# Optimization experiments

Measured on AMD Instinct MI355X. Metric: run time of the kernel, lower is better.

The kernel has to match this reference:

```python
import jax, jax.numpy as jnp
import numpy as np


def _normalize_xyz_with_pc(pc, xyz):
    # Center by point-cloud centroid, scale by max radius of centered cloud.
    center = pc.mean(axis=1, keepdims=True)                      # [B,1,3]
    pc_c = pc - center
    scale = jnp.sqrt((pc_c ** 2).sum(-1)).max(axis=1)            # [B]
    scale = jnp.maximum(scale, 1e-6)[:, None, None]              # [B,1,1]
    return (xyz - center) / scale


def _nn_gather(seed_n, pts_n, feat):
    # seed_n [B,M,3], pts_n [B,K,3], feat [B,C,K] -> [B,C,M]
    d2 = ((seed_n ** 2).sum(-1)[:, :, None]
          + (pts_n ** 2).sum(-1)[:, None, :]
          - 2.0 * jnp.einsum('bmd,bkd->bmk', seed_n, pts_n))     # [B,M,K]
    idx = jnp.argmin(d2, axis=-1)                                # [B,M]
    return jnp.take_along_axis(feat, idx[:, None, :], axis=2)    # [B,C,M]


def _conv1x1(w, b, x):
    # w [O,C], b [O], x [B,C,M] -> [B,O,M]
    return jnp.einsum('oc,bcm->bom', w, x) + b[None, :, None]


def setup_inputs() -> dict:
    key = jax.random.key(0)
    ks = jax.random.split(key, 10)
    B, N, M, K, D = 4, 20000, 1024, 16384, 768
    return {
        'point_cloud': jax.random.normal(ks[0], (B, N, 3), jnp.float32),
        'seed_xyz': jax.random.normal(ks[1], (B, M, 3), jnp.float32),
        'seed_features': jax.random.normal(ks[2], (B, 256, M), jnp.float32),
        'pts': jax.random.normal(ks[3], (B, K, 3), jnp.float32),
        'feat': jax.random.normal(ks[4], (B, D, K), jnp.float32),
        'ln_gamma': jnp.ones((D,), jnp.float32),
        'ln_beta': jnp.zeros((D,), jnp.float32),
        'pw1': jax.random.normal(ks[5], (256, D), jnp.float32) * 0.02,
        'pb1': jnp.zeros((256,), jnp.float32),
        'pw2': jax.random.normal(ks[6], (256, 256), jnp.float32) * 0.02,
        'pb2': jnp.zeros((256,), jnp.float32),
        'fw1': jax.random.normal(ks[7], (256, 512), jnp.float32) * 0.02,
        'fb1': jnp.zeros((256,), jnp.float32),
        'fw2': jax.random.normal(ks[8], (256, 256), jnp.float32) * 0.02,
        'fb2': jnp.zeros((256,), jnp.float32),
    }


def reference(point_cloud, seed_xyz, seed_features, pts, feat,
              ln_gamma, ln_beta, pw1, pb1, pw2, pb2, fw1, fb1, fw2, fb2):
    seed_n = _normalize_xyz_with_pc(point_cloud, seed_xyz)       # [B,M,3]
    pts_n = _normalize_xyz_with_pc(point_cloud, pts)             # [B,K,3]
    vggt_raw = _nn_gather(seed_n, pts_n, feat)                   # [B,768,M]

    # LayerNorm over channel dim (applied on [B,M,768] in the original)
    x = vggt_raw.transpose(0, 2, 1)                              # [B,M,768]
    mu = x.mean(-1, keepdims=True)
    var = x.var(-1, keepdims=True)
    x_ln = ((x - mu) * jax.lax.rsqrt(var + 1e-5) * ln_gamma + ln_beta)
    x_ln = x_ln.transpose(0, 2, 1)                               # [B,768,M]

    vggt_proj = _conv1x1(pw2, pb2, jax.nn.relu(_conv1x1(pw1, pb1, x_ln)))
    fused = jnp.concatenate([seed_features, vggt_proj], axis=1)  # [B,512,M]
    mixed = _conv1x1(fw2, fb2, jax.nn.relu(_conv1x1(fw1, fb1, fused)))
    return mixed                                                 # [B,256,M]
```

## Files before the change

### kernel.cpp

```cpp
#include <hip/hip_runtime.h>
#include <math.h>

#define B_ 4
#define N_ 20000
#define M_ 1024
#define K_ 16384
#define D_ 768

typedef __attribute__((ext_vector_type(8))) short bf16x8;
typedef __attribute__((ext_vector_type(4))) float f32x4;

#define OFF_PART   0ul
#define OFF_RAD    1024ul
#define OFF_IDX    4096ul
#define OFF_P4     32768ul
#define OFF_G      2097152ul
#define OFF_XLN    16777216ul
#define OFF_FUSED  25165824ul
#define OFF_H2     29360128ul
#define OFF_WB1    33554432ul
#define OFF_WCAT   34603008ul
#define OFF_WB4    35651584ul
#define OFF_BC     36700160ul

__device__ inline unsigned short f2bf(float x) {
    union { float f; unsigned int u; } v; v.f = x;
    unsigned int r = v.u + 0x7fffu + ((v.u >> 16) & 1u);
    return (unsigned short)(r >> 16);
}

__device__ inline void gload_lds16(const void* g, void* lds) {
    __builtin_amdgcn_global_load_lds(
        (const __attribute__((address_space(1))) unsigned int*)g,
        (__attribute__((address_space(3))) unsigned int*)lds, 16, 0, 0);
}

__global__ __launch_bounds__(256) void k_cs_sum(const float* __restrict__ pc,
                                                float* __restrict__ part)
{
    int blk = blockIdx.x, b = blk >> 4, pi = blk & 15;
    const float* p = pc + (size_t)b * N_ * 3;
    int tid = threadIdx.x;
    int i0 = pi * 1250;
    float sx = 0.f, sy = 0.f, sz = 0.f;
    for (int i = i0 + tid; i < i0 + 1250; i += 256) {
        sx += p[i*3+0]; sy += p[i*3+1]; sz += p[i*3+2];
    }
    for (int off = 32; off; off >>= 1) {
        sx += __shfl_down(sx, off, 64);
        sy += __shfl_down(sy, off, 64);
        sz += __shfl_down(sz, off, 64);
    }
    __shared__ float red[3][4];
    int w = tid >> 6, l = tid & 63;
    if (!l) { red[0][w] = sx; red[1][w] = sy; red[2][w] = sz; }
    __syncthreads();
    if (!tid) {
        part[(b*16+pi)*3+0] = red[0][0]+red[0][1]+red[0][2]+red[0][3];
        part[(b*16+pi)*3+1] = red[1][0]+red[1][1]+red[1][2]+red[1][3];
        part[(b*16+pi)*3+2] = red[2][0]+red[2][1]+red[2][2]+red[2][3];
    }
}

__device__ inline void reduce_center(const float* part, int b,
                                     float& cx, float& cy, float& cz)
{
    cx = 0.f; cy = 0.f; cz = 0.f;
    #pragma unroll
    for (int r = 0; r < 16; ++r) {
        cx += part[(b*16+r)*3+0];
        cy += part[(b*16+r)*3+1];
        cz += part[(b*16+r)*3+2];
    }
    cx *= (1.f/N_); cy *= (1.f/N_); cz *= (1.f/N_);
}

__global__ __launch_bounds__(256) void k_cs_rad(const float* __restrict__ pc,
                                                const float* __restrict__ part,
                                                float* __restrict__ rad)
{
    int blk = blockIdx.x, b = blk >> 4, pi = blk & 15;
    float cx, cy, cz;
    reduce_center(part, b, cx, cy, cz);
    const float* p = pc + (size_t)b * N_ * 3;
    int tid = threadIdx.x;
    int i0 = pi * 1250;
    float mx = 0.f;
    for (int i = i0 + tid; i < i0 + 1250; i += 256) {
        float dx = p[i*3+0]-cx, dy = p[i*3+1]-cy, dz = p[i*3+2]-cz;
        mx = fmaxf(mx, dx*dx + dy*dy + dz*dz);
    }
    for (int off = 32; off; off >>= 1) mx = fmaxf(mx, __shfl_down(mx, off, 64));
    __shared__ float red[4];
    int w = tid >> 6, l = tid & 63;
    if (!l) red[w] = mx;
    __syncthreads();
    if (!tid) rad[b*16+pi] = fmaxf(fmaxf(red[0], red[1]), fmaxf(red[2], red[3]));
}

__device__ inline float reduce_scale(const float* rad, int b)
{
    float m = 0.f;
    #pragma unroll
    for (int r = 0; r < 16; ++r) m = fmaxf(m, rad[b*16+r]);
    return fmaxf(sqrtf(m), 1e-6f);
}

__global__ __launch_bounds__(256) void k_prep_pts(const float* __restrict__ pts,
                                                  const float* __restrict__ part,
                                                  const float* __restrict__ rad,
                                                  float4* __restrict__ P4)
{
    int blk = blockIdx.x, b = blk >> 6;
    float cx, cy, cz;
    reduce_center(part, b, cx, cy, cz);
    float sc = 1.f / reduce_scale(rad, b);
    int k = (blk & 63)*256 + threadIdx.x;
    const float* pp = pts + ((size_t)b*K_ + k)*3;
    float px = (pp[0]-cx)*sc, py = (pp[1]-cy)*sc, pz = (pp[2]-cz)*sc;
    P4[(size_t)b*K_ + k] = make_float4(px, py, pz, px*px + py*py + pz*pz);
}

__global__ __launch_bounds__(256) void k_nn(const float* __restrict__ seed_xyz,
                                            const float4* __restrict__ P4,
                                            const float* __restrict__ part,
                                            const float* __restrict__ rad,
                                            int* __restrict__ idx)
{
    int blk = blockIdx.x, b = blk >> 7, g = blk & 127;
    float cx, cy, cz;
    reduce_center(part, b, cx, cy, cz);
    float sc = 1.f / reduce_scale(rad, b);
    int t = threadIdx.x;
    int j = t & 31, s = t >> 5;
    int m = g*8 + s;
    const float* sp = seed_xyz + ((size_t)b*M_ + m)*3;
    float sx = (sp[0]-cx)*sc, sy = (sp[1]-cy)*sc, sz = (sp[2]-cz)*sc;
    float ssq = sx*sx + sy*sy + sz*sz;
    const float4* Pb = P4 + (size_t)b*K_;

    float best[4] = {3.4e38f, 3.4e38f, 3.4e38f, 3.4e38f};
    int   bk[4]   = {0, 0, 0, 0};
    for (int i = 0; i < 512; i += 4) {
        #pragma unroll
        for (int r = 0; r < 4; ++r) {
            int k = (i + r)*32 + j;
            float4 q = Pb[k];
            float d2 = ssq + q.w - 2.f*(sx*q.x + sy*q.y + sz*q.z);
            if (d2 < best[r]) { best[r] = d2; bk[r] = k; }
        }
    }
    float bm = best[0]; int bmk = bk[0];
    #pragma unroll
    for (int r = 1; r < 4; ++r) {
        if (best[r] < bm || (best[r] == bm && bk[r] < bmk)) { bm = best[r]; bmk = bk[r]; }
    }
    #pragma unroll
    for (int mask = 16; mask; mask >>= 1) {
        float ob = __shfl_xor(bm, mask, 64);
        int   ok = __shfl_xor(bmk, mask, 64);
        if (ob < bm || (ob == bm && ok < bmk)) { bm = ob; bmk = ok; }
    }
    if (j == 0) idx[b*M_ + m] = bmk;
}

__global__ __launch_bounds__(256) void k_gather(const float* __restrict__ feat,
                                                const int* __restrict__ idx,
                                                float* __restrict__ G)
{
    int c = blockIdx.x, b = blockIdx.y;
    int t = threadIdx.x;
    const float* frow = feat + ((size_t)b*D_ + c) * K_;
    const int* ib = idx + b*M_;
    float* grow = G + ((size_t)b*D_ + c) * M_;
    #pragma unroll
    for (int r = 0; r < 4; ++r) {
        int m = r*256 + t;
        grow[m] = frow[ib[m]];
    }
}

__global__ __launch_bounds__(256) void k_ln_fused(const float* __restrict__ G,
                                                  const float* __restrict__ gamma,
                                                  const float* __restrict__ beta,
                                                  unsigned short* __restrict__ xln)
{
    int b = blockIdx.y, m0 = blockIdx.x * 32;
    int t = threadIdx.x;
    int ml = t & 31, cp = t >> 5;
    const float* Gb = G + (size_t)b * D_ * M_;
    float s = 0.f, q = 0.f;
    for (int c = cp; c < D_; c += 8) {
        float v = Gb[(size_t)c*M_ + m0 + ml];
        s += v; q += v*v;
    }
    __shared__ float sred[8][32], qred[8][32];
    __shared__ float mu[32], iv[32];
    sred[cp][ml] = s; qred[cp][ml] = q;
    __syncthreads();
    if (t < 32) {
        float S = 0.f, Q = 0.f;
        #pragma unroll
        for (int r = 0; r < 8; ++r) { S += sred[r][t]; Q += qred[r][t]; }
        float m_ = S * (1.f/768.f);
        mu[t] = m_;
        iv[t] = rsqrtf(Q * (1.f/768.f) - m_*m_ + 1e-5f);
    }
    __syncthreads();

    __shared__ float tile[64][33];
    int ty = t >> 5;
    int cx2 = t & 31;
    for (int c0 = 0; c0 < D_; c0 += 64) {
        __syncthreads();
        #pragma unroll
        for (int ri = 0; ri < 8; ++ri) {
            int cl = ty*8 + ri;
            tile[cl][ml] = Gb[(size_t)(c0+cl)*M_ + m0 + ml];
        }
        __syncthreads();
        float2 ga = *(const float2*)&gamma[c0 + 2*cx2];
        float2 be = *(const float2*)&beta[c0 + 2*cx2];
        #pragma unroll
        for (int ri = 0; ri < 4; ++ri) {
            int m_l = ty*4 + ri;
            float v0 = (tile[2*cx2+0][m_l] - mu[m_l]) * iv[m_l] * ga.x + be.x;
            float v1 = (tile[2*cx2+1][m_l] - mu[m_l]) * iv[m_l] * ga.y + be.y;
            ushort2 pk = make_ushort2(f2bf(v0), f2bf(v1));
            *(ushort2*)&xln[((size_t)((b<<10) + m0 + m_l))*D_ + c0 + 2*cx2] = pk;
        }
    }
}

__global__ void k_transpose_sf(const float* __restrict__ sf,
                               unsigned short* __restrict__ fused)
{
    __shared__ float tile[32][33];
    int m0 = blockIdx.x*32, c0 = blockIdx.y*32, b = blockIdx.z;
    int tx = threadIdx.x, ty = threadIdx.y;
    #pragma unroll
    for (int r = 0; r < 32; r += 8)
        tile[ty+r][tx] = sf[((size_t)b*256 + c0+ty+r)*M_ + m0 + tx];
    __syncthreads();
    #pragma unroll
    for (int r = 0; r < 32; r += 8)
        fused[((size_t)(b*M_ + m0+ty+r))*512 + c0 + tx] = f2bf(tile[tx][ty+r]);
}

__global__ __launch_bounds__(256) void k_cvt(const float* __restrict__ pw1,
                                             const float* __restrict__ fw1,
                                             const float* __restrict__ fw2,
                                             unsigned short* __restrict__ Wb1,
                                             unsigned short* __restrict__ Wcat,
                                             unsigned short* __restrict__ Wb4)
{
    int i = blockIdx.x*256 + threadIdx.x;
    Wb1[i] = f2bf(pw1[i]);
    if (i < 65536) {
        int o = i >> 8, c = i & 255;
        Wcat[(size_t)o*512 + c] = f2bf(fw1[(size_t)o*512 + c]);
        Wb4[i] = f2bf(fw2[i]);
    }
}

__global__ __launch_bounds__(256) void k_wc(const float* __restrict__ fw1,
                                            const float* __restrict__ pw2,
                                            const float* __restrict__ pb2,
                                            const float* __restrict__ fb1,
                                            unsigned short* __restrict__ Wcat,
                                            float* __restrict__ bc)
{
    int o = blockIdx.x, t = threadIdx.x;
    const float* fb = fw1 + (size_t)o*512 + 256;
    float acc = 0.f;
    for (int j = 0; j < 256; ++j)
        acc = fmaf(fb[j], pw2[(size_t)j*256 + t], acc);
    Wcat[(size_t)o*512 + 256 + t] = f2bf(acc);
    float v = fb[t] * pb2[t];
    for (int off = 32; off; off >>= 1) v += __shfl_down(v, off, 64);
    __shared__ float red[4];
    if (!(t & 63)) red[t >> 6] = v;
    __syncthreads();
    if (!t) bc[o] = red[0]+red[1]+red[2]+red[3] + fb1[o];
}

__global__ __launch_bounds__(256) void k_gemm_mfma(
    const unsigned short* __restrict__ X, const unsigned short* __restrict__ W,
    const float* __restrict__ bias, int Kdim, int relu, int mode,
    unsigned short* __restrict__ Ybf, int rowStride, int colOff,
    float* __restrict__ Yf)
{
    __shared__ unsigned short Al[64*64];
    __shared__ unsigned short Wl[64*64];
    int t = threadIdx.x, l = t & 63, w = t >> 6;
    int m0 = blockIdx.x * 64, o0 = blockIdx.y * 64;
    f32x4 acc[4];
    #pragma unroll
    for (int j = 0; j < 4; ++j) acc[j] = (f32x4){0.f, 0.f, 0.f, 0.f};

    for (int kc = 0; kc < Kdim; kc += 64) {
        #pragma unroll
        for (int i = 0; i < 2; ++i) {
            int lin = i*4096 + w*1024;
            int lb  = lin + l*16;
            int row = lb >> 7;
            int k16 = (lb >> 4) & 7;
            int ks  = k16 ^ (row & 7);
            gload_lds16(X + (size_t)(m0+row)*Kdim + kc + ks*8, (char*)Al + lin);
            gload_lds16(W + (size_t)(o0+row)*Kdim + kc + ks*8, (char*)Wl + lin);
        }
        __syncthreads();
        #pragma unroll
        for (int kk = 0; kk < 2; ++kk) {
            int arow = w*16 + (l & 15);
            int h = l >> 4;
            bf16x8 a = *(const bf16x8*)&Al[arow*64 + (((kk<<2)|h) ^ (arow & 7))*8];
            #pragma unroll
            for (int j = 0; j < 4; ++j) {
                int orow = j*16 + (l & 15);
                bf16x8 bfr = *(const bf16x8*)&Wl[orow*64 + (((kk<<2)|h) ^ (orow & 7))*8];
                acc[j] = __builtin_amdgcn_mfma_f32_16x16x32_bf16(a, bfr, acc[j], 0, 0, 0);
            }
        }
        __syncthreads();
    }

    int mbase = m0 + w*16 + (l >> 4)*4;
    if (mode == 0) {
        #pragma unroll
        for (int j = 0; j < 4; ++j) {
            int o = o0 + j*16 + (l & 15);
            float bi = bias[o];
            #pragma unroll
            for (int r = 0; r < 4; ++r) {
                float v = acc[j][r] + bi;
                if (relu) v = fmaxf(v, 0.f);
                Ybf[(size_t)(mbase + r)*rowStride + colOff + o] = f2bf(v);
            }
        }
    } else {
        int b = mbase >> 10, ml = mbase & 1023;
        #pragma unroll
        for (int j = 0; j < 4; ++j) {
            int o = o0 + j*16 + (l & 15);
            float bi = bias[o];
            float4 sv = make_float4(acc[j][0]+bi, acc[j][1]+bi, acc[j][2]+bi, acc[j][3]+bi);
            *(float4*)&Yf[((size_t)(b*256 + o))*1024 + ml] = sv;
        }
    }
}

extern "C" void kernel_launch(void* const* d_in, const int* in_sizes, int n_in,
                              void* d_out, int out_size, void* d_ws, size_t ws_size,
                              hipStream_t stream)
{
    (void)in_sizes; (void)n_in; (void)out_size; (void)ws_size;
    const float* pc        = (const float*)d_in[0];
    const float* seed_xyz  = (const float*)d_in[1];
    const float* seed_feat = (const float*)d_in[2];
    const float* pts       = (const float*)d_in[3];
    const float* feat      = (const float*)d_in[4];
    const float* ln_g      = (const float*)d_in[5];
    const float* ln_b      = (const float*)d_in[6];
    const float* pw1       = (const float*)d_in[7];
    const float* pb1       = (const float*)d_in[8];
    const float* pw2       = (const float*)d_in[9];
    const float* pb2       = (const float*)d_in[10];
    const float* fw1       = (const float*)d_in[11];
    const float* fb1       = (const float*)d_in[12];
    const float* fw2       = (const float*)d_in[13];
    const float* fb2       = (const float*)d_in[14];
    float* out = (float*)d_out;

    char* ws = (char*)d_ws;
    float*          part  = (float*)(ws + OFF_PART);
    float*          rad   = (float*)(ws + OFF_RAD);
    int*            idx   = (int*)(ws + OFF_IDX);
    float4*         P4    = (float4*)(ws + OFF_P4);
    float*          G     = (float*)(ws + OFF_G);
    unsigned short* xln   = (unsigned short*)(ws + OFF_XLN);
    unsigned short* fused = (unsigned short*)(ws + OFF_FUSED);
    unsigned short* h2    = (unsigned short*)(ws + OFF_H2);
    unsigned short* Wb1   = (unsigned short*)(ws + OFF_WB1);
    unsigned short* Wcat  = (unsigned short*)(ws + OFF_WCAT);
    unsigned short* Wb4   = (unsigned short*)(ws + OFF_WB4);
    float*          bc    = (float*)(ws + OFF_BC);

    k_cvt<<<768, 256, 0, stream>>>(pw1, fw1, fw2, Wb1, Wcat, Wb4);
    k_wc<<<256, 256, 0, stream>>>(fw1, pw2, pb2, fb1, Wcat, bc);
    k_cs_sum<<<64, 256, 0, stream>>>(pc, part);
    k_cs_rad<<<64, 256, 0, stream>>>(pc, part, rad);
    k_prep_pts<<<256, 256, 0, stream>>>(pts, part, rad, P4);
    k_nn<<<512, 256, 0, stream>>>(seed_xyz, P4, part, rad, idx);
    k_gather<<<dim3(D_, B_), 256, 0, stream>>>(feat, idx, G);
    k_ln_fused<<<dim3(M_/32, B_), 256, 0, stream>>>(G, ln_g, ln_b, xln);
    k_gemm_mfma<<<dim3(64, 4), 256, 0, stream>>>(xln, Wb1, pb1, 768, 1, 0, fused, 512, 256, nullptr);
    k_transpose_sf<<<dim3(M_/32, 256/32, B_), dim3(32, 8), 0, stream>>>(seed_feat, fused);
    k_gemm_mfma<<<dim3(64, 4), 256, 0, stream>>>(fused, Wcat, bc, 512, 1, 0, h2, 256, 0, nullptr);
    k_gemm_mfma<<<dim3(64, 4), 256, 0, stream>>>(h2, Wb4, fb2, 256, 0, 1, nullptr, 0, 0, out);
}
```

Measured before the change: 164.7 us.

## Merge all stages into one cooperative persistent kernel with grid syncs

Result: slower. 345.2 us (+109.6%).

```diff
diff --git a/kernel.cpp b/kernel.cpp
--- a/kernel.cpp
+++ b/kernel.cpp
@@ -1,5 +1,8 @@
 #include <hip/hip_runtime.h>
+#include <hip/hip_cooperative_groups.h>
 #include <math.h>
+
+namespace cg = cooperative_groups;
 
 #define B_ 4
 #define N_ 20000
@@ -13,7 +16,6 @@
 #define OFF_PART   0ul
 #define OFF_RAD    1024ul
 #define OFF_IDX    4096ul
-#define OFF_P4     32768ul
 #define OFF_G      2097152ul
 #define OFF_XLN    16777216ul
 #define OFF_FUSED  25165824ul
@@ -35,32 +37,13 @@
         (__attribute__((address_space(3))) unsigned int*)lds, 16, 0, 0);
 }
 
-__global__ __launch_bounds__(256) void k_cs_sum(const float* __restrict__ pc,
-                                                float* __restrict__ part)
-{
-    int blk = blockIdx.x, b = blk >> 4, pi = blk & 15;
-    const float* p = pc + (size_t)b * N_ * 3;
-    int tid = threadIdx.x;
-    int i0 = pi * 1250;
-    float sx = 0.f, sy = 0.f, sz = 0.f;
-    for (int i = i0 + tid; i < i0 + 1250; i += 256) {
-        sx += p[i*3+0]; sy += p[i*3+1]; sz += p[i*3+2];
-    }
-    for (int off = 32; off; off >>= 1) {
-        sx += __shfl_down(sx, off, 64);
-        sy += __shfl_down(sy, off, 64);
-        sz += __shfl_down(sz, off, 64);
-    }
-    __shared__ float red[3][4];
-    int w = tid >> 6, l = tid & 63;
-    if (!l) { red[0][w] = sx; red[1][w] = sy; red[2][w] = sz; }
-    __syncthreads();
-    if (!tid) {
-        part[(b*16+pi)*3+0] = red[0][0]+red[0][1]+red[0][2]+red[0][3];
-        part[(b*16+pi)*3+1] = red[1][0]+red[1][1]+red[1][2]+red[1][3];
-        part[(b*16+pi)*3+2] = red[2][0]+red[2][1]+red[2][2]+red[2][3];
-    }
-}
+struct MegaArgs {
+    const float *pc, *seed_xyz, *sf, *pts, *feat, *ln_g, *ln_b;
+    const float *pw1, *pb1, *pw2, *pb2, *fw1, *fb1, *fw2, *fb2;
+    float *part; float *rad; int *idx; float *G;
+    unsigned short *xln, *fused, *h2, *Wb1, *Wcat, *Wb4;
+    float *bc; float *out;
+};
 
 __device__ inline void reduce_center(const float* part, int b,
                                      float& cx, float& cy, float& cz)
@@ -75,29 +58,6 @@
     cx *= (1.f/N_); cy *= (1.f/N_); cz *= (1.f/N_);
 }
 
-__global__ __launch_bounds__(256) void k_cs_rad(const float* __restrict__ pc,
-                                                const float* __restrict__ part,
-                                                float* __restrict__ rad)
-{
-    int blk = blockIdx.x, b = blk >> 4, pi = blk & 15;
-    float cx, cy, cz;
-    reduce_center(part, b, cx, cy, cz);
-    const float* p = pc + (size_t)b * N_ * 3;
-    int tid = threadIdx.x;
-    int i0 = pi * 1250;
-    float mx = 0.f;
-    for (int i = i0 + tid; i < i0 + 1250; i += 256) {
-        float dx = p[i*3+0]-cx, dy = p[i*3+1]-cy, dz = p[i*3+2]-cz;
-        mx = fmaxf(mx, dx*dx + dy*dy + dz*dz);
-    }
-    for (int off = 32; off; off >>= 1) mx = fmaxf(mx, __shfl_down(mx, off, 64));
-    __shared__ float red[4];
-    int w = tid >> 6, l = tid & 63;
-    if (!l) red[w] = mx;
-    __syncthreads();
-    if (!tid) rad[b*16+pi] = fmaxf(fmaxf(red[0], red[1]), fmaxf(red[2], red[3]));
-}
-
 __device__ inline float reduce_scale(const float* rad, int b)
 {
     float m = 0.f;
@@ -106,194 +66,15 @@
     return fmaxf(sqrtf(m), 1e-6f);
 }
 
-__global__ __launch_bounds__(256) void k_prep_pts(const float* __restrict__ pts,
-                                                  const float* __restrict__ part,
-                                                  const float* __restrict__ rad,
-                                                  float4* __restrict__ P4)
-{
-    int blk = blockIdx.x, b = blk >> 6;
-    float cx, cy, cz;
-    reduce_center(part, b, cx, cy, cz);
-    float sc = 1.f / reduce_scale(rad, b);
-    int k = (blk & 63)*256 + threadIdx.x;
-    const float* pp = pts + ((size_t)b*K_ + k)*3;
-    float px = (pp[0]-cx)*sc, py = (pp[1]-cy)*sc, pz = (pp[2]-cz)*sc;
-    P4[(size_t)b*K_ + k] = make_float4(px, py, pz, px*px + py*py + pz*pz);
-}
-
-__global__ __launch_bounds__(256) void k_nn(const float* __restrict__ seed_xyz,
-                                            const float4* __restrict__ P4,
-                                            const float* __restrict__ part,
-                                            const float* __restrict__ rad,
-                                            int* __restrict__ idx)
-{
-    int blk = blockIdx.x, b = blk >> 7, g = blk & 127;
-    float cx, cy, cz;
-    reduce_center(part, b, cx, cy, cz);
-    float sc = 1.f / reduce_scale(rad, b);
-    int t = threadIdx.x;
-    int j = t & 31, s = t >> 5;
-    int m = g*8 + s;
-    const float* sp = seed_xyz + ((size_t)b*M_ + m)*3;
-    float sx = (sp[0]-cx)*sc, sy = (sp[1]-cy)*sc, sz = (sp[2]-cz)*sc;
-    float ssq = sx*sx + sy*sy + sz*sz;
-    const float4* Pb = P4 + (size_t)b*K_;
-
-    float best[4] = {3.4e38f, 3.4e38f, 3.4e38f, 3.4e38f};
-    int   bk[4]   = {0, 0, 0, 0};
-    for (int i = 0; i < 512; i += 4) {
-        #pragma unroll
-        for (int r = 0; r < 4; ++r) {
-            int k = (i + r)*32 + j;
-            float4 q = Pb[k];
-            float d2 = ssq + q.w - 2.f*(sx*q.x + sy*q.y + sz*q.z);
-            if (d2 < best[r]) { best[r] = d2; bk[r] = k; }
-        }
-    }
-    float bm = best[0]; int bmk = bk[0];
-    #pragma unroll
-    for (int r = 1; r < 4; ++r) {
-        if (best[r] < bm || (best[r] == bm && bk[r] < bmk)) { bm = best[r]; bmk = bk[r]; }
-    }
-    #pragma unroll
-    for (int mask = 16; mask; mask >>= 1) {
-        float ob = __shfl_xor(bm, mask, 64);
-        int   ok = __shfl_xor(bmk, mask, 64);
-        if (ob < bm || (ob == bm && ok < bmk)) { bm = ob; bmk = ok; }
-    }
-    if (j == 0) idx[b*M_ + m] = bmk;
-}
-
-__global__ __launch_bounds__(256) void k_gather(const float* __restrict__ feat,
-                                                const int* __restrict__ idx,
-                                                float* __restrict__ G)
-{
-    int c = blockIdx.x, b = blockIdx.y;
-    int t = threadIdx.x;
-    const float* frow = feat + ((size_t)b*D_ + c) * K_;
-    const int* ib = idx + b*M_;
-    float* grow = G + ((size_t)b*D_ + c) * M_;
-    #pragma unroll
-    for (int r = 0; r < 4; ++r) {
-        int m = r*256 + t;
-        grow[m] = frow[ib[m]];
-    }
-}
-
-__global__ __launch_bounds__(256) void k_ln_fused(const float* __restrict__ G,
-                                                  const float* __restrict__ gamma,
-                                                  const float* __restrict__ beta,
-                                                  unsigned short* __restrict__ xln)
-{
-    int b = blockIdx.y, m0 = blockIdx.x * 32;
-    int t = threadIdx.x;
-    int ml = t & 31, cp = t >> 5;
-    const float* Gb = G + (size_t)b * D_ * M_;
-    float s = 0.f, q = 0.f;
-    for (int c = cp; c < D_; c += 8) {
-        float v = Gb[(size_t)c*M_ + m0 + ml];
-        s += v; q += v*v;
-    }
-    __shared__ float sred[8][32], qred[8][32];
-    __shared__ float mu[32], iv[32];
-    sred[cp][ml] = s; qred[cp][ml] = q;
-    __syncthreads();
-    if (t < 32) {
-        float S = 0.f, Q = 0.f;
-        #pragma unroll
-        for (int r = 0; r < 8; ++r) { S += sred[r][t]; Q += qred[r][t]; }
-        float m_ = S * (1.f/768.f);
-        mu[t] = m_;
-        iv[t] = rsqrtf(Q * (1.f/768.f) - m_*m_ + 1e-5f);
-    }
-    __syncthreads();
-
-    __shared__ float tile[64][33];
-    int ty = t >> 5;
-    int cx2 = t & 31;
-    for (int c0 = 0; c0 < D_; c0 += 64) {
-        __syncthreads();
-        #pragma unroll
-        for (int ri = 0; ri < 8; ++ri) {
-            int cl = ty*8 + ri;
-            tile[cl][ml] = Gb[(size_t)(c0+cl)*M_ + m0 + ml];
-        }
-        __syncthreads();
-        float2 ga = *(const float2*)&gamma[c0 + 2*cx2];
-        float2 be = *(const float2*)&beta[c0 + 2*cx2];
-        #pragma unroll
-        for (int ri = 0; ri < 4; ++ri) {
-            int m_l = ty*4 + ri;
-            float v0 = (tile[2*cx2+0][m_l] - mu[m_l]) * iv[m_l] * ga.x + be.x;
-            float v1 = (tile[2*cx2+1][m_l] - mu[m_l]) * iv[m_l] * ga.y + be.y;
-            ushort2 pk = make_ushort2(f2bf(v0), f2bf(v1));
-            *(ushort2*)&xln[((size_t)((b<<10) + m0 + m_l))*D_ + c0 + 2*cx2] = pk;
-        }
-    }
-}
-
-__global__ void k_transpose_sf(const float* __restrict__ sf,
-                               unsigned short* __restrict__ fused)
-{
-    __shared__ float tile[32][33];
-    int m0 = blockIdx.x*32, c0 = blockIdx.y*32, b = blockIdx.z;
-    int tx = threadIdx.x, ty = threadIdx.y;
-    #pragma unroll
-    for (int r = 0; r < 32; r += 8)
-        tile[ty+r][tx] = sf[((size_t)b*256 + c0+ty+r)*M_ + m0 + tx];
-    __syncthreads();
-    #pragma unroll
-    for (int r = 0; r < 32; r += 8)
-        fused[((size_t)(b*M_ + m0+ty+r))*512 + c0 + tx] = f2bf(tile[tx][ty+r]);
-}
-
-__global__ __launch_bounds__(256) void k_cvt(const float* __restrict__ pw1,
-                                             const float* __restrict__ fw1,
-                                             const float* __restrict__ fw2,
-                                             unsigned short* __restrict__ Wb1,
-                                             unsigned short* __restrict__ Wcat,
-                                             unsigned short* __restrict__ Wb4)
-{
-    int i = blockIdx.x*256 + threadIdx.x;
-    Wb1[i] = f2bf(pw1[i]);
-    if (i < 65536) {
-        int o = i >> 8, c = i & 255;
-        Wcat[(size_t)o*512 + c] = f2bf(fw1[(size_t)o*512 + c]);
-        Wb4[i] = f2bf(fw2[i]);
-    }
-}
-
-__global__ __launch_bounds__(256) void k_wc(const float* __restrict__ fw1,
-                                            const float* __restrict__ pw2,
-                                            const float* __restrict__ pb2,
-                                            const float* __restrict__ fb1,
-                                            unsigned short* __restrict__ Wcat,
-                                            float* __restrict__ bc)
-{
-    int o = blockIdx.x, t = threadIdx.x;
-    const float* fb = fw1 + (size_t)o*512 + 256;
-    float acc = 0.f;
-    for (int j = 0; j < 256; ++j)
-        acc = fmaf(fb[j], pw2[(size_t)j*256 + t], acc);
-    Wcat[(size_t)o*512 + 256 + t] = f2bf(acc);
-    float v = fb[t] * pb2[t];
-    for (int off = 32; off; off >>= 1) v += __shfl_down(v, off, 64);
-    __shared__ float red[4];
-    if (!(t & 63)) red[t >> 6] = v;
-    __syncthreads();
-    if (!t) bc[o] = red[0]+red[1]+red[2]+red[3] + fb1[o];
-}
-
-__global__ __launch_bounds__(256) void k_gemm_mfma(
-    const unsigned short* __restrict__ X, const unsigned short* __restrict__ W,
-    const float* __restrict__ bias, int Kdim, int relu, int mode,
-    unsigned short* __restrict__ Ybf, int rowStride, int colOff,
-    float* __restrict__ Yf)
-{
-    __shared__ unsigned short Al[64*64];
-    __shared__ unsigned short Wl[64*64];
-    int t = threadIdx.x, l = t & 63, w = t >> 6;
-    int m0 = blockIdx.x * 64, o0 = blockIdx.y * 64;
+__device__ void gemm_phase(const unsigned short* X, const unsigned short* W,
+                           const float* bias, int Kdim, int relu, int mode,
+                           unsigned short* Ybf, int rowStride, int colOff,
+                           float* Yf, char* smem, int bid, int t)
+{
+    unsigned short* Al = (unsigned short*)smem;
+    unsigned short* Wl = (unsigned short*)(smem + 8192);
+    int l = t & 63, w = t >> 6;
+    int m0 = (bid & 63) * 64, o0 = (bid >> 6) * 64;
     f32x4 acc[4];
     #pragma unroll
     for (int j = 0; j < 4; ++j) acc[j] = (f32x4){0.f, 0.f, 0.f, 0.f};
@@ -350,52 +131,247 @@
     }
 }
 
+__global__ __launch_bounds__(256) void k_mega(MegaArgs a)
+{
+    __shared__ __align__(16) char smem[52224];
+    __shared__ float sred[16][16];
+    __shared__ float qred[16][16];
+    __shared__ float smu[16], siv[16];
+    __shared__ float wred[4];
+    __shared__ float csred[3][4];
+
+    cg::grid_group grid = cg::this_grid();
+    int bid = blockIdx.x, t = threadIdx.x;
+    int lane = t & 63, wv = t >> 6;
+
+    {
+        int i0 = bid*256 + t;
+        for (int i = i0; i < 256*768; i += 65536) a.Wb1[i] = f2bf(a.pw1[i]);
+        int o = i0 >> 8, c = i0 & 255;
+        a.Wcat[(size_t)o*512 + c] = f2bf(a.fw1[(size_t)o*512 + c]);
+        a.Wb4[i0] = f2bf(a.fw2[i0]);
+    }
+    {
+        const float* fb = a.fw1 + (size_t)bid*512 + 256;
+        float acc = 0.f;
+        for (int j = 0; j < 256; ++j)
+            acc = fmaf(fb[j], a.pw2[j*256 + t], acc);
+        a.Wcat[(size_t)bid*512 + 256 + t] = f2bf(acc);
+        float v = fb[t] * a.pb2[t];
+        for (int off = 32; off; off >>= 1) v += __shfl_down(v, off, 64);
+        if (!lane) wred[wv] = v;
+        __syncthreads();
+        if (!t) a.bc[bid] = wred[0]+wred[1]+wred[2]+wred[3] + a.fb1[bid];
+    }
+    if (bid < 64) {
+        int b = bid >> 4, pi = bid & 15;
+        const float* p = a.pc + (size_t)b * N_ * 3;
+        int i0 = pi * 1250;
+        float sx = 0.f, sy = 0.f, sz = 0.f;
+        for (int i = i0 + t; i < i0 + 1250; i += 256) {
+            sx += p[i*3+0]; sy += p[i*3+1]; sz += p[i*3+2];
+        }
+        for (int off = 32; off; off >>= 1) {
+            sx += __shfl_down(sx, off, 64);
+            sy += __shfl_down(sy, off, 64);
+            sz += __shfl_down(sz, off, 64);
+        }
+        if (!lane) { csred[0][wv] = sx; csred[1][wv] = sy; csred[2][wv] = sz; }
+        __syncthreads();
+        if (!t) {
+            a.part[(b*16+pi)*3+0] = csred[0][0]+csred[0][1]+csred[0][2]+csred[0][3];
+            a.part[(b*16+pi)*3+1] = csred[1][0]+csred[1][1]+csred[1][2]+csred[1][3];
+            a.part[(b*16+pi)*3+2] = csred[2][0]+csred[2][1]+csred[2][2]+csred[2][3];
+        }
+    }
+    {
+        float (*tile)[33] = (float(*)[33])smem;
+        int tx = t & 31, ty = t >> 5;
+        for (int r = 0; r < 4; ++r) {
+            int id = bid*4 + r;
+            int b = id >> 8, rem = id & 255;
+            int m0 = (rem & 31) * 32, c0 = (rem >> 5) * 32;
+            __syncthreads();
+            #pragma unroll
+            for (int rr = 0; rr < 32; rr += 8)
+                tile[ty+rr][tx] = a.sf[((size_t)b*256 + c0+ty+rr)*M_ + m0 + tx];
+            __syncthreads();
+            #pragma unroll
+            for (int rr = 0; rr < 32; rr += 8)
+                a.fused[((size_t)(b*M_ + m0+ty+rr))*512 + c0 + tx] = f2bf(tile[tx][ty+rr]);
+        }
+    }
+    grid.sync();
+
+    if (bid < 64) {
+        int b = bid >> 4, pi = bid & 15;
+        float cx, cy, cz;
+        reduce_center(a.part, b, cx, cy, cz);
+        const float* p = a.pc + (size_t)b * N_ * 3;
+        int i0 = pi * 1250;
+        float mx = 0.f;
+        for (int i = i0 + t; i < i0 + 1250; i += 256) {
+            float dx = p[i*3+0]-cx, dy = p[i*3+1]-cy, dz = p[i*3+2]-cz;
+            mx = fmaxf(mx, dx*dx + dy*dy + dz*dz);
+        }
+        for (int off = 32; off; off >>= 1) mx = fmaxf(mx, __shfl_down(mx, off, 64));
+        if (!lane) wred[wv] = mx;
+        __syncthreads();
+        if (!t) a.rad[b*16+pi] = fmaxf(fmaxf(wred[0], wred[1]), fmaxf(wred[2], wred[3]));
+    }
+    grid.sync();
+
+    {
+        int b = bid >> 6, sgrp = bid & 63;
+        float cx, cy, cz;
+        reduce_center(a.part, b, cx, cy, cz);
+        float scinv = 1.f / reduce_scale(a.rad, b);
+        int j = t & 15, s = t >> 4;
+        int m = sgrp*16 + s;
+        const float* sp = a.seed_xyz + ((size_t)b*M_ + m)*3;
+        float sx = (sp[0]-cx)*scinv, sy = (sp[1]-cy)*scinv, sz = (sp[2]-cz)*scinv;
+        float ssq = sx*sx + sy*sy + sz*sz;
+        const float* pb = a.pts + (size_t)b*K_*3;
+        float4* P = (float4*)smem;
+
+        float bestv[4] = {3.4e38f, 3.4e38f, 3.4e38f, 3.4e38f};
+        int   bestk[4] = {0, 0, 0, 0};
+        for (int c0 = 0; c0 < K_; c0 += 1024) {
+            __syncthreads();
+            #pragma unroll
+            for (int r = 0; r < 4; ++r) {
+                int k = c0 + r*256 + t;
+                const float* pp = pb + (size_t)k*3;
+                float px = (pp[0]-cx)*scinv, py = (pp[1]-cy)*scinv, pz = (pp[2]-cz)*scinv;
+                P[r*256+t] = make_float4(px, py, pz, px*px + py*py + pz*pz);
+            }
+            __syncthreads();
+            for (int u = 0; u < 64; u += 4) {
+                #pragma unroll
+                for (int r = 0; r < 4; ++r) {
+                    int ti = (u+r)*16 + j;
+                    float4 q = P[ti];
+                    float d2 = ssq + q.w - 2.f*(sx*q.x + sy*q.y + sz*q.z);
+                    int k = c0 + ti;
+                    if (d2 < bestv[r]) { bestv[r] = d2; bestk[r] = k; }
+                }
+            }
+        }
+        float bm = bestv[0]; int bmk = bestk[0];
+        #pragma unroll
+        for (int r = 1; r < 4; ++r)
+            if (bestv[r] < bm || (bestv[r] == bm && bestk[r] < bmk)) { bm = bestv[r]; bmk = bestk[r]; }
+        #pragma unroll
+        for (int mask = 8; mask; mask >>= 1) {
+            float ob = __shfl_xor(bm, mask, 64);
+            int   ok = __shfl_xor(bmk, mask, 64);
+            if (ob < bm || (ob == bm && ok < bmk)) { bm = ob; bmk = ok; }
+        }
+        if (j == 0) a.idx[b*M_ + m] = bmk;
+    }
+    grid.sync();
+
+    {
+        for (int u = 0; u < 12; ++u) {
+            int row = bid*12 + u;
+            int b = row / 768, c = row - b*768;
+            const float* frow = a.feat + ((size_t)b*D_ + c) * K_;
+            const int* ib = a.idx + b*M_;
+            float* grow = a.G + ((size_t)b*D_ + c) * M_;
+            #pragma unroll
+            for (int r = 0; r < 4; ++r) {
+                int m = r*256 + t;
+                grow[m] = frow[ib[m]];
+            }
+        }
+    }
+    grid.sync();
+
+    {
+        int b = bid >> 6, m0 = (bid & 63) * 16;
+        const float* Gb = a.G + (size_t)b * D_ * M_;
+        float (*L)[17] = (float(*)[17])smem;
+        #pragma unroll 4
+        for (int u = 0; u < 48; ++u) {
+            int lin = u*256 + t;
+            int c = lin >> 4, ml = lin & 15;
+            L[c][ml] = Gb[(size_t)c*M_ + m0 + ml];
+        }
+        __syncthreads();
+        int m = t & 15, seg = t >> 4;
+        float s = 0.f, q = 0.f;
+        for (int i = 0; i < 48; ++i) {
+            float v = L[seg*48 + i][m];
+            s += v; q += v*v;
+        }
+        sred[seg][m] = s; qred[seg][m] = q;
+        __syncthreads();
+        if (t < 16) {
+            float S = 0.f, Q = 0.f;
+            #pragma unroll
+            for (int r = 0; r < 16; ++r) { S += sred[r][t]; Q += qred[r][t]; }
+            float mu = S * (1.f/768.f);
+            smu[t] = mu;
+            siv[t] = rsqrtf(Q * (1.f/768.f) - mu*mu + 1e-5f);
+        }
+        __syncthreads();
+        float mu = smu[m], iv = siv[m];
+        size_t orow = ((size_t)(b*M_ + m0 + m)) * D_;
+        for (int i = 0; i < 48; i += 2) {
+            int c = seg*48 + i;
+            float v0 = (L[c][m]   - mu) * iv * a.ln_g[c]   + a.ln_b[c];
+            float v1 = (L[c+1][m] - mu) * iv * a.ln_g[c+1] + a.ln_b[c+1];
+            ushort2 pk = make_ushort2(f2bf(v0), f2bf(v1));
+            *(ushort2*)&a.xln[orow + c] = pk;
+        }
+    }
+    grid.sync();
+
+    gemm_phase(a.xln, a.Wb1, a.pb1, 768, 1, 0, a.fused, 512, 256, nullptr, smem, bid, t);
+    grid.sync();
+
+    gemm_phase(a.fused, a.Wcat, a.bc, 512, 1, 0, a.h2, 256, 0, nullptr, smem, bid, t);
+    grid.sync();
+
+    gemm_phase(a.h2, a.Wb4, a.fb2, 256, 0, 1, nullptr, 0, 0, a.out, smem, bid, t);
+}
+
 extern "C" void kernel_launch(void* const* d_in, const int* in_sizes, int n_in,
                               void* d_out, int out_size, void* d_ws, size_t ws_size,
                               hipStream_t stream)
 {
     (void)in_sizes; (void)n_in; (void)out_size; (void)ws_size;
-    const float* pc        = (const float*)d_in[0];
-    const float* seed_xyz  = (const float*)d_in[1];
-    const float* seed_feat = (const float*)d_in[2];
-    const float* pts       = (const float*)d_in[3];
-    const float* feat      = (const float*)d_in[4];
-    const float* ln_g      = (const float*)d_in[5];
-    const float* ln_b      = (const float*)d_in[6];
-    const float* pw1       = (const float*)d_in[7];
-    const float* pb1       = (const float*)d_in[8];
-    const float* pw2       = (const float*)d_in[9];
-    const float* pb2       = (const float*)d_in[10];
-    const float* fw1       = (const float*)d_in[11];
-    const float* fb1       = (const float*)d_in[12];
-    const float* fw2       = (const float*)d_in[13];
-    const float* fb2       = (const float*)d_in[14];
-    float* out = (float*)d_out;
-
     char* ws = (char*)d_ws;
-    float*          part  = (float*)(ws + OFF_PART);
-    float*          rad   = (float*)(ws + OFF_RAD);
-    int*            idx   = (int*)(ws + OFF_IDX);
-    float4*         P4    = (float4*)(ws + OFF_P4);
-    float*          G     = (float*)(ws + OFF_G);
-    unsigned short* xln   = (unsigned short*)(ws + OFF_XLN);
-    unsigned short* fused = (unsigned short*)(ws + OFF_FUSED);
-    unsigned short* h2    = (unsigned short*)(ws + OFF_H2);
-    unsigned short* Wb1   = (unsigned short*)(ws + OFF_WB1);
-    unsigned short* Wcat  = (unsigned short*)(ws + OFF_WCAT);
-    unsigned short* Wb4   = (unsigned short*)(ws + OFF_WB4);
-    float*          bc    = (float*)(ws + OFF_BC);
-
-    k_cvt<<<768, 256, 0, stream>>>(pw1, fw1, fw2, Wb1, Wcat, Wb4);
-    k_wc<<<256, 256, 0, stream>>>(fw1, pw2, pb2, fb1, Wcat, bc);
-    k_cs_sum<<<64, 256, 0, stream>>>(pc, part);
-    k_cs_rad<<<64, 256, 0, stream>>>(pc, part, rad);
-    k_prep_pts<<<256, 256, 0, stream>>>(pts, part, rad, P4);
-    k_nn<<<512, 256, 0, stream>>>(seed_xyz, P4, part, rad, idx);
-    k_gather<<<dim3(D_, B_), 256, 0, stream>>>(feat, idx, G);
-    k_ln_fused<<<dim3(M_/32, B_), 256, 0, stream>>>(G, ln_g, ln_b, xln);
-    k_gemm_mfma<<<dim3(64, 4), 256, 0, stream>>>(xln, Wb1, pb1, 768, 1, 0, fused, 512, 256, nullptr);
-    k_transpose_sf<<<dim3(M_/32, 256/32, B_), dim3(32, 8), 0, stream>>>(seed_feat, fused);
-    k_gemm_mfma<<<dim3(64, 4), 256, 0, stream>>>(fused, Wcat, bc, 512, 1, 0, h2, 256, 0, nullptr);
-    k_gemm_mfma<<<dim3(64, 4), 256, 0, stream>>>(h2, Wb4, fb2, 256, 0, 1, nullptr, 0, 0, out);
-}
+    MegaArgs a;
+    a.pc       = (const float*)d_in[0];
+    a.seed_xyz = (const float*)d_in[1];
+    a.sf       = (const float*)d_in[2];
+    a.pts      = (const float*)d_in[3];
+    a.feat     = (const float*)d_in[4];
+    a.ln_g     = (const float*)d_in[5];
+    a.ln_b     = (const float*)d_in[6];
+    a.pw1      = (const float*)d_in[7];
+    a.pb1      = (const float*)d_in[8];
+    a.pw2      = (const float*)d_in[9];
+    a.pb2      = (const float*)d_in[10];
+    a.fw1      = (const float*)d_in[11];
+    a.fb1      = (const float*)d_in[12];
+    a.fw2      = (const float*)d_in[13];
+    a.fb2      = (const float*)d_in[14];
+    a.part  = (float*)(ws + OFF_PART);
+    a.rad   = (float*)(ws + OFF_RAD);
+    a.idx   = (int*)(ws + OFF_IDX);
+    a.G     = (float*)(ws + OFF_G);
+    a.xln   = (unsigned short*)(ws + OFF_XLN);
+    a.fused = (unsigned short*)(ws + OFF_FUSED);
+    a.h2    = (unsigned short*)(ws + OFF_H2);
+    a.Wb1   = (unsigned short*)(ws + OFF_WB1);
+    a.Wcat  = (unsigned short*)(ws + OFF_WCAT);
+    a.Wb4   = (unsigned short*)(ws + OFF_WB4);
+    a.bc    = (float*)(ws + OFF_BC);
+    a.out   = (float*)d_out;
+
+    void* kargs[] = { &a };
+    hipLaunchCooperativeKernel((const void*)k_mega, dim3(256), dim3(256),
+                               kargs, 0, stream);
+}
```

## Merge small prep kernels and inline point normalization into NN search

Applied to the files above, without the earlier changes.

New measurement: 163.7 us. No clear change (-0.7%).

```diff
diff --git a/kernel.cpp b/kernel.cpp
--- a/kernel.cpp
+++ b/kernel.cpp
@@ -13,7 +13,6 @@
 #define OFF_PART   0ul
 #define OFF_RAD    1024ul
 #define OFF_IDX    4096ul
-#define OFF_P4     32768ul
 #define OFF_G      2097152ul
 #define OFF_XLN    16777216ul
 #define OFF_FUSED  25165824ul
@@ -35,33 +34,6 @@
         (__attribute__((address_space(3))) unsigned int*)lds, 16, 0, 0);
 }
 
-__global__ __launch_bounds__(256) void k_cs_sum(const float* __restrict__ pc,
-                                                float* __restrict__ part)
-{
-    int blk = blockIdx.x, b = blk >> 4, pi = blk & 15;
-    const float* p = pc + (size_t)b * N_ * 3;
-    int tid = threadIdx.x;
-    int i0 = pi * 1250;
-    float sx = 0.f, sy = 0.f, sz = 0.f;
-    for (int i = i0 + tid; i < i0 + 1250; i += 256) {
-        sx += p[i*3+0]; sy += p[i*3+1]; sz += p[i*3+2];
-    }
-    for (int off = 32; off; off >>= 1) {
-        sx += __shfl_down(sx, off, 64);
-        sy += __shfl_down(sy, off, 64);
-        sz += __shfl_down(sz, off, 64);
-    }
-    __shared__ float red[3][4];
-    int w = tid >> 6, l = tid & 63;
-    if (!l) { red[0][w] = sx; red[1][w] = sy; red[2][w] = sz; }
-    __syncthreads();
-    if (!tid) {
-        part[(b*16+pi)*3+0] = red[0][0]+red[0][1]+red[0][2]+red[0][3];
-        part[(b*16+pi)*3+1] = red[1][0]+red[1][1]+red[1][2]+red[1][3];
-        part[(b*16+pi)*3+2] = red[2][0]+red[2][1]+red[2][2]+red[2][3];
-    }
-}
-
 __device__ inline void reduce_center(const float* part, int b,
                                      float& cx, float& cy, float& cz)
 {
@@ -73,6 +45,72 @@
         cz += part[(b*16+r)*3+2];
     }
     cx *= (1.f/N_); cy *= (1.f/N_); cz *= (1.f/N_);
+}
+
+__device__ inline float reduce_scale(const float* rad, int b)
+{
+    float m = 0.f;
+    #pragma unroll
+    for (int r = 0; r < 16; ++r) m = fmaxf(m, rad[b*16+r]);
+    return fmaxf(sqrtf(m), 1e-6f);
+}
+
+__global__ __launch_bounds__(256) void k_pre(
+    const float* __restrict__ pc,
+    const float* __restrict__ pw1, const float* __restrict__ pw2,
+    const float* __restrict__ pb2,
+    const float* __restrict__ fw1, const float* __restrict__ fb1,
+    const float* __restrict__ fw2,
+    unsigned short* __restrict__ Wb1, unsigned short* __restrict__ Wcat,
+    unsigned short* __restrict__ Wb4, float* __restrict__ bc,
+    float* __restrict__ part)
+{
+    int bid = blockIdx.x, t = threadIdx.x;
+    int lane = t & 63, wv = t >> 6;
+    __shared__ float red[3][4];
+
+    if (bid < 768) {
+        int i0 = bid*256 + t;
+        Wb1[i0] = f2bf(pw1[i0]);
+        if (i0 < 65536) {
+            int o = i0 >> 8, c = i0 & 255;
+            Wcat[(size_t)o*512 + c] = f2bf(fw1[(size_t)o*512 + c]);
+            Wb4[i0] = f2bf(fw2[i0]);
+        }
+    }
+    if (bid < 256) {
+        const float* fb = fw1 + (size_t)bid*512 + 256;
+        float acc = 0.f;
+        for (int j = 0; j < 256; ++j)
+            acc = fmaf(fb[j], pw2[j*256 + t], acc);
+        Wcat[(size_t)bid*512 + 256 + t] = f2bf(acc);
+        float v = fb[t] * pb2[t];
+        for (int off = 32; off; off >>= 1) v += __shfl_down(v, off, 64);
+        if (!lane) red[0][wv] = v;
+        __syncthreads();
+        if (!t) bc[bid] = red[0][0]+red[0][1]+red[0][2]+red[0][3] + fb1[bid];
+    } else if (bid >= 768) {
+        int pi = bid - 768;
+        int b = pi >> 4, chunk = pi & 15;
+        const float* p = pc + (size_t)b * N_ * 3;
+        int i0 = chunk * 1250;
+        float sx = 0.f, sy = 0.f, sz = 0.f;
+        for (int i = i0 + t; i < i0 + 1250; i += 256) {
+            sx += p[i*3+0]; sy += p[i*3+1]; sz += p[i*3+2];
+        }
+        for (int off = 32; off; off >>= 1) {
+            sx += __shfl_down(sx, off, 64);
+            sy += __shfl_down(sy, off, 64);
+            sz += __shfl_down(sz, off, 64);
+        }
+        if (!lane) { red[0][wv] = sx; red[1][wv] = sy; red[2][wv] = sz; }
+        __syncthreads();
+        if (!t) {
+            part[(b*16+chunk)*3+0] = red[0][0]+red[0][1]+red[0][2]+red[0][3];
+            part[(b*16+chunk)*3+1] = red[1][0]+red[1][1]+red[1][2]+red[1][3];
+            part[(b*16+chunk)*3+2] = red[2][0]+red[2][1]+red[2][2]+red[2][3];
+        }
+    }
 }
 
 __global__ __launch_bounds__(256) void k_cs_rad(const float* __restrict__ pc,
@@ -98,31 +136,8 @@
     if (!tid) rad[b*16+pi] = fmaxf(fmaxf(red[0], red[1]), fmaxf(red[2], red[3]));
 }
 
-__device__ inline float reduce_scale(const float* rad, int b)
-{
-    float m = 0.f;
-    #pragma unroll
-    for (int r = 0; r < 16; ++r) m = fmaxf(m, rad[b*16+r]);
-    return fmaxf(sqrtf(m), 1e-6f);
-}
-
-__global__ __launch_bounds__(256) void k_prep_pts(const float* __restrict__ pts,
-                                                  const float* __restrict__ part,
-                                                  const float* __restrict__ rad,
-                                                  float4* __restrict__ P4)
-{
-    int blk = blockIdx.x, b = blk >> 6;
-    float cx, cy, cz;
-    reduce_center(part, b, cx, cy, cz);
-    float sc = 1.f / reduce_scale(rad, b);
-    int k = (blk & 63)*256 + threadIdx.x;
-    const float* pp = pts + ((size_t)b*K_ + k)*3;
-    float px = (pp[0]-cx)*sc, py = (pp[1]-cy)*sc, pz = (pp[2]-cz)*sc;
-    P4[(size_t)b*K_ + k] = make_float4(px, py, pz, px*px + py*py + pz*pz);
-}
-
 __global__ __launch_bounds__(256) void k_nn(const float* __restrict__ seed_xyz,
-                                            const float4* __restrict__ P4,
+                                            const float* __restrict__ pts,
                                             const float* __restrict__ part,
                                             const float* __restrict__ rad,
                                             int* __restrict__ idx)
@@ -130,14 +145,14 @@
     int blk = blockIdx.x, b = blk >> 7, g = blk & 127;
     float cx, cy, cz;
     reduce_center(part, b, cx, cy, cz);
-    float sc = 1.f / reduce_scale(rad, b);
+    float scinv = 1.f / reduce_scale(rad, b);
     int t = threadIdx.x;
     int j = t & 31, s = t >> 5;
     int m = g*8 + s;
     const float* sp = seed_xyz + ((size_t)b*M_ + m)*3;
-    float sx = (sp[0]-cx)*sc, sy = (sp[1]-cy)*sc, sz = (sp[2]-cz)*sc;
+    float sx = (sp[0]-cx)*scinv, sy = (sp[1]-cy)*scinv, sz = (sp[2]-cz)*scinv;
     float ssq = sx*sx + sy*sy + sz*sz;
-    const float4* Pb = P4 + (size_t)b*K_;
+    const float* pb = pts + (size_t)b*K_*3;
 
     float best[4] = {3.4e38f, 3.4e38f, 3.4e38f, 3.4e38f};
     int   bk[4]   = {0, 0, 0, 0};
@@ -145,8 +160,10 @@
         #pragma unroll
         for (int r = 0; r < 4; ++r) {
             int k = (i + r)*32 + j;
-            float4 q = Pb[k];
-            float d2 = ssq + q.w - 2.f*(sx*q.x + sy*q.y + sz*q.z);
+            const float* pp = pb + (size_t)k*3;
+            float px = (pp[0]-cx)*scinv, py = (pp[1]-cy)*scinv, pz = (pp[2]-cz)*scinv;
+            float qw = px*px + py*py + pz*pz;
+            float d2 = ssq + qw - 2.f*(sx*px + sy*py + sz*pz);
             if (d2 < best[r]) { best[r] = d2; bk[r] = k; }
         }
     }
@@ -164,19 +181,36 @@
     if (j == 0) idx[b*M_ + m] = bmk;
 }
 
-__global__ __launch_bounds__(256) void k_gather(const float* __restrict__ feat,
-                                                const int* __restrict__ idx,
-                                                float* __restrict__ G)
-{
-    int c = blockIdx.x, b = blockIdx.y;
-    int t = threadIdx.x;
-    const float* frow = feat + ((size_t)b*D_ + c) * K_;
-    const int* ib = idx + b*M_;
-    float* grow = G + ((size_t)b*D_ + c) * M_;
-    #pragma unroll
-    for (int r = 0; r < 4; ++r) {
-        int m = r*256 + t;
-        grow[m] = frow[ib[m]];
+__global__ __launch_bounds__(256) void k_gather_tsf(const float* __restrict__ feat,
+                                                    const int* __restrict__ idx,
+                                                    const float* __restrict__ sf,
+                                                    float* __restrict__ G,
+                                                    unsigned short* __restrict__ fused)
+{
+    int bid = blockIdx.x, t = threadIdx.x;
+    if (bid < 3072) {
+        int b = bid / 768, c = bid - b*768;
+        const float* frow = feat + ((size_t)b*D_ + c) * K_;
+        const int* ib = idx + b*M_;
+        float* grow = G + ((size_t)b*D_ + c) * M_;
+        #pragma unroll
+        for (int r = 0; r < 4; ++r) {
+            int m = r*256 + t;
+            grow[m] = frow[ib[m]];
+        }
+    } else {
+        __shared__ float tile[32][33];
+        int id = bid - 3072;
+        int b = id >> 8, rem = id & 255;
+        int m0 = (rem & 31) * 32, c0 = (rem >> 5) * 32;
+        int tx = t & 31, ty = t >> 5;
+        #pragma unroll
+        for (int rr = 0; rr < 32; rr += 8)
+            tile[ty+rr][tx] = sf[((size_t)b*256 + c0+ty+rr)*M_ + m0 + tx];
+        __syncthreads();
+        #pragma unroll
+        for (int rr = 0; rr < 32; rr += 8)
+            fused[((size_t)(b*M_ + m0+ty+rr))*512 + c0 + tx] = f2bf(tile[tx][ty+rr]);
     }
 }
 
@@ -230,58 +264,6 @@
             *(ushort2*)&xln[((size_t)((b<<10) + m0 + m_l))*D_ + c0 + 2*cx2] = pk;
         }
     }
-}
-
-__global__ void k_transpose_sf(const float* __restrict__ sf,
-                               unsigned short* __restrict__ fused)
-{
-    __shared__ float tile[32][33];
-    int m0 = blockIdx.x*32, c0 = blockIdx.y*32, b = blockIdx.z;
-    int tx = threadIdx.x, ty = threadIdx.y;
-    #pragma unroll
-    for (int r = 0; r < 32; r += 8)
-        tile[ty+r][tx] = sf[((size_t)b*256 + c0+ty+r)*M_ + m0 + tx];
-    __syncthreads();
-    #pragma unroll
-    for (int r = 0; r < 32; r += 8)
-        fused[((size_t)(b*M_ + m0+ty+r))*512 + c0 + tx] = f2bf(tile[tx][ty+r]);
-}
-
-__global__ __launch_bounds__(256) void k_cvt(const float* __restrict__ pw1,
-                                             const float* __restrict__ fw1,
-                                             const float* __restrict__ fw2,
-                                             unsigned short* __restrict__ Wb1,
-                                             unsigned short* __restrict__ Wcat,
-                                             unsigned short* __restrict__ Wb4)
-{
-    int i = blockIdx.x*256 + threadIdx.x;
-    Wb1[i] = f2bf(pw1[i]);
-    if (i < 65536) {
-        int o = i >> 8, c = i & 255;
-        Wcat[(size_t)o*512 + c] = f2bf(fw1[(size_t)o*512 + c]);
-        Wb4[i] = f2bf(fw2[i]);
-    }
-}
-
-__global__ __launch_bounds__(256) void k_wc(const float* __restrict__ fw1,
-                                            const float* __restrict__ pw2,
-                                            const float* __restrict__ pb2,
-                                            const float* __restrict__ fb1,
-                                            unsigned short* __restrict__ Wcat,
-                                            float* __restrict__ bc)
-{
-    int o = blockIdx.x, t = threadIdx.x;
-    const float* fb = fw1 + (size_t)o*512 + 256;
-    float acc = 0.f;
-    for (int j = 0; j < 256; ++j)
-        acc = fmaf(fb[j], pw2[(size_t)j*256 + t], acc);
-    Wcat[(size_t)o*512 + 256 + t] = f2bf(acc);
-    float v = fb[t] * pb2[t];
-    for (int off = 32; off; off >>= 1) v += __shfl_down(v, off, 64);
-    __shared__ float red[4];
-    if (!(t & 63)) red[t >> 6] = v;
-    __syncthreads();
-    if (!t) bc[o] = red[0]+red[1]+red[2]+red[3] + fb1[o];
 }
 
 __global__ __launch_bounds__(256) void k_gemm_mfma(
@@ -376,7 +358,6 @@
     float*          part  = (float*)(ws + OFF_PART);
     float*          rad   = (float*)(ws + OFF_RAD);
     int*            idx   = (int*)(ws + OFF_IDX);
-    float4*         P4    = (float4*)(ws + OFF_P4);
     float*          G     = (float*)(ws + OFF_G);
     unsigned short* xln   = (unsigned short*)(ws + OFF_XLN);
     unsigned short* fused = (unsigned short*)(ws + OFF_FUSED);
@@ -386,16 +367,13 @@
     unsigned short* Wb4   = (unsigned short*)(ws + OFF_WB4);
     float*          bc    = (float*)(ws + OFF_BC);
 
-    k_cvt<<<768, 256, 0, stream>>>(pw1, fw1, fw2, Wb1, Wcat, Wb4);
-    k_wc<<<256, 256, 0, stream>>>(fw1, pw2, pb2, fb1, Wcat, bc);
-    k_cs_sum<<<64, 256, 0, stream>>>(pc, part);
+    k_pre<<<832, 256, 0, stream>>>(pc, pw1, pw2, pb2, fw1, fb1, fw2,
+                                   Wb1, Wcat, Wb4, bc, part);
     k_cs_rad<<<64, 256, 0, stream>>>(pc, part, rad);
-    k_prep_pts<<<256, 256, 0, stream>>>(pts, part, rad, P4);
-    k_nn<<<512, 256, 0, stream>>>(seed_xyz, P4, part, rad, idx);
-    k_gather<<<dim3(D_, B_), 256, 0, stream>>>(feat, idx, G);
+    k_nn<<<512, 256, 0, stream>>>(seed_xyz, pts, part, rad, idx);
+    k_gather_tsf<<<4096, 256, 0, stream>>>(feat, idx, seed_feat, G, fused);
     k_ln_fused<<<dim3(M_/32, B_), 256, 0, stream>>>(G, ln_g, ln_b, xln);
     k_gemm_mfma<<<dim3(64, 4), 256, 0, stream>>>(xln, Wb1, pb1, 768, 1, 0, fused, 512, 256, nullptr);
-    k_transpose_sf<<<dim3(M_/32, 256/32, B_), dim3(32, 8), 0, stream>>>(seed_feat, fused);
     k_gemm_mfma<<<dim3(64, 4), 256, 0, stream>>>(fused, Wcat, bc, 512, 1, 0, h2, 256, 0, nullptr);
     k_gemm_mfma<<<dim3(64, 4), 256, 0, stream>>>(h2, Wb4, fb2, 256, 0, 1, nullptr, 0, 0, out);
 }
```
